# Optimization experiments

Measured on AMD Instinct MI355X. Metric: run time of the kernel, lower is better.

The kernel has to match this reference:

```python
import jax, jax.numpy as jnp
import numpy as np

B, T, D, A = 8, 256, 512, 512  # hidden dim D must equal attn size A per the TF code


def setup_inputs() -> dict:
    key = jax.random.key(0)
    ks = jax.random.split(key, 12)
    g = lambda k, shp, fan: jax.random.normal(k, shp, jnp.float32) * (1.0 / np.sqrt(fan))
    return {
        "state_outputs": jax.random.normal(ks[0], (B, T, D), jnp.float32),
        "final_state": jax.random.normal(ks[1], (B, D), jnp.float32),
        "intent_v": g(ks[2], (A,), A),
        "W_ih": g(ks[3], (D, A), D), "b_ih": jnp.zeros((A,), jnp.float32),
        "W_ii": g(ks[4], (D, A), D), "b_ii": jnp.zeros((A,), jnp.float32),
        "slot_v": g(ks[5], (A,), A),
        "W_sh": g(ks[6], (D, A), D), "b_sh": jnp.zeros((A,), jnp.float32),
        "W_si": g(ks[7], (D, A), D), "b_si": jnp.zeros((A,), jnp.float32),
    }


def reference(state_outputs, final_state, intent_v, W_ih, b_ih, W_ii, b_ii,
              slot_v, W_sh, b_sh, W_si, b_si):
    # ---- intent attention ----
    ih = jnp.einsum('btd,da->bta', state_outputs, W_ih) + b_ih        # [B,T,A]
    ii = final_state @ W_ii + b_ii                                     # [B,A]
    intent_score = jnp.sum(intent_v * jnp.tanh(ih + ii[:, None, :]), axis=-1)  # [B,T]
    intent_w = jax.nn.softmax(intent_score, axis=-1)
    c_intent = jnp.einsum('bt,btd->bd', intent_w, state_outputs)       # [B,D]

    # ---- slot attention ----
    sh = jnp.einsum('btd,da->bta', state_outputs, W_sh) + b_sh         # keys   [B,T,A]
    si = jnp.einsum('btd,da->bta', state_outputs, W_si) + b_si         # queries[B,T,A]
    # score[b,t,s] over pairs: tanh(sh[b,s] + si[b,t]) . slot_v
    slot_score = jnp.sum(slot_v * jnp.tanh(sh[:, None, :, :] + si[:, :, None, :]), axis=-1)  # [B,T,T]
    slot_w = jax.nn.softmax(slot_score, axis=-1)
    c_slot = jnp.einsum('bts,bsd->btd', slot_w, state_outputs)         # [B,T,D]
    return c_slot, c_intent
```

## Files before the change

kernel.cpp:

```cpp
#include <hip/hip_runtime.h>

#define BB 8
#define TT 256
#define DD 512
#define AA 512

#define PS 2.8853900817779268f
#define LOG2E 1.4426950408889634f

typedef __attribute__((ext_vector_type(8))) short short8;
typedef __attribute__((ext_vector_type(4))) float f32x4;

__device__ __forceinline__ float fast_tanh(float x) {
    float e = __builtin_amdgcn_exp2f(x * PS);
    float r = __builtin_amdgcn_rcpf(1.0f + e);
    return fmaf(-2.0f, r, 1.0f);
}

__device__ __forceinline__ ushort f2bf(float x) {
    uint u = __float_as_uint(x);
    uint r = (u + 0x7fffu + ((u >> 16) & 1u)) >> 16;
    return (ushort)r;
}
__device__ __forceinline__ float bf2f(ushort h) {
    return __uint_as_float(((uint)h) << 16);
}

__global__ __launch_bounds__(256) void prep(const float* __restrict__ SO,
                                            ushort* __restrict__ Ast,
                                            const float* __restrict__ Wsh,
                                            const float* __restrict__ Wsi,
                                            const float* __restrict__ Wih,
                                            ushort* __restrict__ Wt,
                                            const float* __restrict__ fs_g,
                                            const float* __restrict__ Wii,
                                            const float* __restrict__ bii,
                                            float* __restrict__ ii) {
    const int bid = blockIdx.x;
    const int tid = threadIdx.x;
    __shared__ float T[32][33];
    __shared__ float fs[DD];

    if (bid < 16) {
        int b = bid >> 1, half = bid & 1;
        int a = half * 256 + tid;
        fs[tid]       = fs_g[b * DD + tid];
        fs[tid + 256] = fs_g[b * DD + tid + 256];
        __syncthreads();
        float acc = bii[a];
        #pragma unroll 8
        for (int d = 0; d < DD; ++d)
            acc = fmaf(fs[d], Wii[(size_t)d * AA + a], acc);
        ii[b * AA + a] = acc;
    } else if (bid < 784) {
        int lbid = bid - 16;
        int z = lbid >> 8;
        int rem = lbid & 255;
        const float* W = (z == 0) ? Wsh : (z == 1) ? Wsi : Wih;
        int k0 = (rem & 15) * 32, n0 = (rem >> 4) * 32;
        int tx = tid & 31, ty = tid >> 5;
        #pragma unroll
        for (int r = 0; r < 4; ++r) {
            int kl = ty * 4 + r;
            T[kl][tx] = W[(size_t)(k0 + kl) * 512 + n0 + tx];
        }
        __syncthreads();
        size_t nbase = (size_t)z * 512 + n0;
        #pragma unroll
        for (int r = 0; r < 4; ++r) {
            int nl = ty * 4 + r;
            float v = T[tx][nl];
            ushort hi = f2bf(v);
            ushort lo = f2bf(v - bf2f(hi));
            Wt[(nbase + nl) * 1024 + k0 + tx]       = hi;
            Wt[(nbase + nl) * 1024 + 512 + k0 + tx] = lo;
        }
    } else {
        int qid = (bid - 784) * 256 + tid;
        int m = qid >> 7;
        int k4 = (qid & 127) * 4;
        float4 v = *reinterpret_cast<const float4*>(&SO[(size_t)m * 512 + k4]);
        ushort4 hi, lo;
        hi.x = f2bf(v.x); lo.x = f2bf(v.x - bf2f(hi.x));
        hi.y = f2bf(v.y); lo.y = f2bf(v.y - bf2f(hi.y));
        hi.z = f2bf(v.z); lo.z = f2bf(v.z - bf2f(hi.z));
        hi.w = f2bf(v.w); lo.w = f2bf(v.w - bf2f(hi.w));
        *reinterpret_cast<ushort4*>(&Ast[(size_t)m * 1024 + k4])       = hi;
        *reinterpret_cast<ushort4*>(&Ast[(size_t)m * 1024 + 512 + k4]) = lo;
    }
}

__global__ __launch_bounds__(256) void gemm_mfma(
    const ushort* __restrict__ Ast, const ushort* __restrict__ Wt,
    const float* __restrict__ bsh, const float* __restrict__ bsi,
    const float* __restrict__ bih,
    const float* __restrict__ ii, const float* __restrict__ iv,
    float* __restrict__ EhT, float* __restrict__ Es, float* __restrict__ ipart) {
    __shared__ __align__(16) ushort Al[2][128 * 32];
    __shared__ __align__(16) ushort Bl[2][128 * 32];
    const int tid = threadIdx.x;
    const int wave = tid >> 6, lane = tid & 63;
    const int wr = wave >> 1, wc = wave & 1;
    const int m0 = blockIdx.x * 128;
    const int by = blockIdx.y;
    const int l15 = lane & 15, kb = lane >> 4;

    f32x4 acc[4][4] = {};

    const char* Ab = reinterpret_cast<const char*>(Ast);
    const char* Bb = reinterpret_cast<const char*>(Wt);
    char* AlB = reinterpret_cast<char*>(&Al[0][0]);
    char* BlB = reinterpret_cast<char*>(&Bl[0][0]);

    const int srow  = tid >> 1;
    const int sslot = (tid & 1) * 2;
    const int swz   = (srow >> 1) & 3;
    const int lw0 = srow * 64 + ((sslot    ) ^ swz) * 16;
    const int lw1 = srow * 64 + ((sslot + 1) ^ swz) * 16;
    const char* agp = Ab + (size_t)(m0 + srow) * 2048 + sslot * 16;
    const char* bgp = Bb + (size_t)(by * 128 + srow) * 2048 + sslot * 16;

    int aro[4], bro[4];
    #pragma unroll
    for (int i = 0; i < 4; ++i) {
        int ra = wr * 64 + i * 16 + l15;
        aro[i] = ra * 64 + ((kb ^ ((ra >> 1) & 3)) * 16);
        int rb = wc * 64 + i * 16 + l15;
        bro[i] = rb * 64 + ((kb ^ ((rb >> 1) & 3)) * 16);
    }

    #define ABYTE(k0) (((k0) < 1024 ? (k0) : (k0) - 1024) * 2)
    #define BBYTE(k0) (((k0) < 512 ? (k0) : (k0) - 512) * 2)

    {
        short8 a0 = *reinterpret_cast<const short8*>(agp + ABYTE(0));
        short8 a1 = *reinterpret_cast<const short8*>(agp + ABYTE(0) + 16);
        short8 b0 = *reinterpret_cast<const short8*>(bgp + BBYTE(0));
        short8 b1 = *reinterpret_cast<const short8*>(bgp + BBYTE(0) + 16);
        *reinterpret_cast<short8*>(AlB + lw0) = a0;
        *reinterpret_cast<short8*>(AlB + lw1) = a1;
        *reinterpret_cast<short8*>(BlB + lw0) = b0;
        *reinterpret_cast<short8*>(BlB + lw1) = b1;
    }
    __syncthreads();

    int cur = 0;
    for (int it = 0; it < 48; ++it) {
        short8 a0, a1, b0, b1;
        const bool pf = (it + 1 < 48);
        if (pf) {
            int k0 = (it + 1) * 32;
            int ab = ABYTE(k0), bb = BBYTE(k0);
            a0 = *reinterpret_cast<const short8*>(agp + ab);
            a1 = *reinterpret_cast<const short8*>(agp + ab + 16);
            b0 = *reinterpret_cast<const short8*>(bgp + bb);
            b1 = *reinterpret_cast<const short8*>(bgp + bb + 16);
        }
        const char* Ac = AlB + cur * 8192;
        const char* Bc = BlB + cur * 8192;
        short8 af[4], bf[4];
        #pragma unroll
        for (int i = 0; i < 4; ++i) {
            af[i] = *reinterpret_cast<const short8*>(Ac + aro[i]);
            bf[i] = *reinterpret_cast<const short8*>(Bc + bro[i]);
        }
        #pragma unroll
        for (int i = 0; i < 4; ++i)
            #pragma unroll
            for (int j = 0; j < 4; ++j)
                acc[i][j] = __builtin_amdgcn_mfma_f32_16x16x32_bf16(
                    af[i], bf[j], acc[i][j], 0, 0, 0);
        if (pf) {
            char* An = AlB + (cur ^ 1) * 8192;
            char* Bn = BlB + (cur ^ 1) * 8192;
            *reinterpret_cast<short8*>(An + lw0) = a0;
            *reinterpret_cast<short8*>(An + lw1) = a1;
            *reinterpret_cast<short8*>(Bn + lw0) = b0;
            *reinterpret_cast<short8*>(Bn + lw1) = b1;
        }
        __syncthreads();
        cur ^= 1;
    }

    const int b = m0 >> 8;
    const int region = by >> 2;
    if (region == 0) {
        #pragma unroll
        for (int i = 0; i < 4; ++i) {
            int t0 = (m0 & 255) + wr * 64 + i * 16 + kb * 4;
            #pragma unroll
            for (int j = 0; j < 4; ++j) {
                int n = by * 128 + wc * 64 + j * 16 + l15;
                float bbv = bsh[n];
                float4 v;
                v.x = __builtin_amdgcn_exp2f((acc[i][j][0] + bbv) * PS);
                v.y = __builtin_amdgcn_exp2f((acc[i][j][1] + bbv) * PS);
                v.z = __builtin_amdgcn_exp2f((acc[i][j][2] + bbv) * PS);
                v.w = __builtin_amdgcn_exp2f((acc[i][j][3] + bbv) * PS);
                *reinterpret_cast<float4*>(&EhT[((size_t)b * 512 + n) * 256 + t0]) = v;
            }
        }
    } else if (region == 1) {
        #pragma unroll
        for (int i = 0; i < 4; ++i) {
            #pragma unroll
            for (int j = 0; j < 4; ++j) {
                int n = (by - 4) * 128 + wc * 64 + j * 16 + l15;
                float bbv = bsi[n];
                #pragma unroll
                for (int r = 0; r < 4; ++r) {
                    int m = m0 + wr * 64 + i * 16 + kb * 4 + r;
                    Es[(size_t)m * 512 + n] = __builtin_amdgcn_exp2f((acc[i][j][r] + bbv) * PS);
                }
            }
        }
    } else {
        int slot = (by - 8) * 2 + wc;
        #pragma unroll
        for (int i = 0; i < 4; ++i) {
            float p0 = 0.f, p1 = 0.f, p2 = 0.f, p3 = 0.f;
            #pragma unroll
            for (int j = 0; j < 4; ++j) {
                int n = (by - 8) * 128 + wc * 64 + j * 16 + l15;
                float add = bih[n] + ii[b * 512 + n];
                float w = iv[n];
                p0 = fmaf(w, fast_tanh(acc[i][j][0] + add), p0);
                p1 = fmaf(w, fast_tanh(acc[i][j][1] + add), p1);
                p2 = fmaf(w, fast_tanh(acc[i][j][2] + add), p2);
                p3 = fmaf(w, fast_tanh(acc[i][j][3] + add), p3);
            }
            #pragma unroll
            for (int off = 1; off < 16; off <<= 1) {
                p0 += __shfl_xor(p0, off);
                p1 += __shfl_xor(p1, off);
                p2 += __shfl_xor(p2, off);
                p3 += __shfl_xor(p3, off);
            }
            int mb = m0 + wr * 64 + i * 16 + kb * 4;
            if (l15 == 0) ipart[slot * 2048 + mb + 0] = p0;
            if (l15 == 1) ipart[slot * 2048 + mb + 1] = p1;
            if (l15 == 2) ipart[slot * 2048 + mb + 2] = p2;
            if (l15 == 3) ipart[slot * 2048 + mb + 3] = p3;
        }
    }
}

#define TS 64
#define KS 16
#define LPAD 72

__global__ __launch_bounds__(256) void k0_ii(const float* __restrict__ fs_g,
                                             const float* __restrict__ Wii,
                                             const float* __restrict__ bii,
                                             float* __restrict__ ii) {
    int b = blockIdx.x, tid = threadIdx.x;
    int a = blockIdx.y * 256 + tid;
    __shared__ float fs[DD];
    fs[tid]       = fs_g[b * DD + tid];
    fs[tid + 256] = fs_g[b * DD + tid + 256];
    __syncthreads();
    float acc = bii[a];
    #pragma unroll 8
    for (int d = 0; d < DD; ++d)
        acc = fmaf(fs[d], Wii[(size_t)d * AA + a], acc);
    ii[b * AA + a] = acc;
}

__global__ __launch_bounds__(256) void k1_gemm_old(
    const float* __restrict__ SO,
    const float* __restrict__ Wsh, const float* __restrict__ bsh,
    const float* __restrict__ Wsi, const float* __restrict__ bsi,
    const float* __restrict__ Wih, const float* __restrict__ bih,
    const float* __restrict__ ii, const float* __restrict__ iv,
    float* __restrict__ EhT, float* __restrict__ Es, float* __restrict__ ipart) {
    const int mode = blockIdx.z;
    const float* W;
    const float* bias;
    if (mode == 0)      { W = Wsh; bias = bsh; }
    else if (mode == 1) { W = Wsi; bias = bsi; }
    else                { W = Wih; bias = bih; }

    const int m0 = blockIdx.x * TS;
    const int n0 = blockIdx.y * TS;
    const int tid = threadIdx.x;
    const int tx = tid & 15, ty = tid >> 4;

    __shared__ __align__(16) float As[KS][LPAD];
    __shared__ __align__(16) float Bs[KS][LPAD];
    __shared__ __align__(16) float Cs[TS][LPAD];

    float acc[4][4] = {};
    const int arow = tid >> 2;
    const int akc  = (tid & 3) * 4;
    const int brw  = tid >> 4;
    const int bnc  = (tid & 15) * 4;

    for (int k0 = 0; k0 < DD; k0 += KS) {
        float4 av = *reinterpret_cast<const float4*>(&SO[(m0 + arow) * DD + k0 + akc]);
        As[akc + 0][arow] = av.x;
        As[akc + 1][arow] = av.y;
        As[akc + 2][arow] = av.z;
        As[akc + 3][arow] = av.w;
        float4 bv = *reinterpret_cast<const float4*>(&W[(k0 + brw) * AA + n0 + bnc]);
        *reinterpret_cast<float4*>(&Bs[brw][bnc]) = bv;
        __syncthreads();
        #pragma unroll
        for (int kk = 0; kk < KS; ++kk) {
            float4 a4 = *reinterpret_cast<const float4*>(&As[kk][ty * 4]);
            float4 b4 = *reinterpret_cast<const float4*>(&Bs[kk][tx * 4]);
            float av_[4] = {a4.x, a4.y, a4.z, a4.w};
            float bv_[4] = {b4.x, b4.y, b4.z, b4.w};
            #pragma unroll
            for (int i = 0; i < 4; ++i)
                #pragma unroll
                for (int j = 0; j < 4; ++j)
                    acc[i][j] = fmaf(av_[i], bv_[j], acc[i][j]);
        }
        __syncthreads();
    }

    if (mode == 1) {
        #pragma unroll
        for (int i = 0; i < 4; ++i) {
            int m = m0 + ty * 4 + i;
            float4 v;
            v.x = __builtin_amdgcn_exp2f((acc[i][0] + bias[n0 + tx * 4 + 0]) * PS);
            v.y = __builtin_amdgcn_exp2f((acc[i][1] + bias[n0 + tx * 4 + 1]) * PS);
            v.z = __builtin_amdgcn_exp2f((acc[i][2] + bias[n0 + tx * 4 + 2]) * PS);
            v.w = __builtin_amdgcn_exp2f((acc[i][3] + bias[n0 + tx * 4 + 3]) * PS);
            *reinterpret_cast<float4*>(&Es[(size_t)m * AA + n0 + tx * 4]) = v;
        }
    } else if (mode == 0) {
        #pragma unroll
        for (int i = 0; i < 4; ++i)
            #pragma unroll
            for (int j = 0; j < 4; ++j)
                Cs[tx * 4 + j][ty * 4 + i] =
                    __builtin_amdgcn_exp2f((acc[i][j] + bias[n0 + tx * 4 + j]) * PS);
        __syncthreads();
        int row = tid >> 2, part = tid & 3;
        int bb = m0 >> 8;
        int tstart = (m0 & 255) + part * 16;
        float* dst = &EhT[bb * (AA * TT) + (n0 + row) * TT + tstart];
        #pragma unroll
        for (int q = 0; q < 4; ++q) {
            float4 v = *reinterpret_cast<const float4*>(&Cs[row][part * 16 + q * 4]);
            *reinterpret_cast<float4*>(&dst[q * 4]) = v;
        }
    } else {
        int bb = m0 >> 8;
        #pragma unroll
        for (int i = 0; i < 4; ++i) {
            float p = 0.f;
            #pragma unroll
            for (int j = 0; j < 4; ++j) {
                int n = n0 + tx * 4 + j;
                float x = acc[i][j] + bias[n] + ii[bb * AA + n];
                p = fmaf(iv[n], fast_tanh(x), p);
            }
            Cs[ty * 4 + i][tx] = p;
        }
        __syncthreads();
        if (tid < 64) {
            float s = 0.f;
            #pragma unroll
            for (int k = 0; k < 16; ++k) s += Cs[tid][k];
            ipart[blockIdx.y * 2048 + m0 + tid] = s;
        }
    }
}

__global__ __launch_bounds__(512) void k3_fused(const float* __restrict__ SO,
                                                const float* __restrict__ EhT,
                                                const float* __restrict__ Es,
                                                const float* __restrict__ sv_g,
                                                const float* __restrict__ ipart,
                                                float* __restrict__ out_cslot,
                                                float* __restrict__ out_cint,
                                                int npart) {
    const int bid = blockIdx.x;
    const int tid = threadIdx.x;

    __shared__ __align__(16) float est[512][4];
    __shared__ __align__(16) float sv[512];
    __shared__ __align__(8)  float yp[4][4][256];
    __shared__ __align__(16) float wlt[256][4];
    __shared__ float redm[4][2];
    __shared__ float reds[4][2];
    __shared__ float redI[256];
    __shared__ float wlI[256];

    if (bid >= 8) {
        const int sb_ = bid - 8;
        const int b = sb_ & 7;
        const int t0 = (sb_ >> 3) * 4;
        const int sp = tid & 127;
        const int ah = tid >> 7;
        const int abase = ah * 128;

        {
            const float* esrc = &Es[(size_t)(b * 256 + t0) * 512];
            #pragma unroll
            for (int i = tid; i < 2048; i += 512) est[i & 511][i >> 9] = esrc[i];
            sv[tid] = sv_g[tid];
        }
        __syncthreads();

        const float* hp = &EhT[((size_t)b * 512 + abase) * 256 + 2 * sp];
        float a00=0.f,a01=0.f,a10=0.f,a11=0.f,a20=0.f,a21=0.f,a30=0.f,a31=0.f;
        for (int a0 = 0; a0 < 128; a0 += 4) {
            float4 v4 = *reinterpret_cast<const float4*>(&sv[abase + a0]);
            float2 h[4];
            #pragma unroll
            for (int u = 0; u < 4; ++u)
                h[u] = *reinterpret_cast<const float2*>(&hp[(a0 + u) * 256]);
            #pragma unroll
            for (int u = 0; u < 4; ++u) {
                float4 e4 = *reinterpret_cast<const float4*>(&est[abase + a0 + u][0]);
                float vv = (u == 0) ? v4.x : (u == 1) ? v4.y : (u == 2) ? v4.z : v4.w;
                float hx = h[u].x, hy = h[u].y;
                a00 = fmaf(vv, __builtin_amdgcn_rcpf(fmaf(hx, e4.x, 1.f)), a00);
                a01 = fmaf(vv, __builtin_amdgcn_rcpf(fmaf(hy, e4.x, 1.f)), a01);
                a10 = fmaf(vv, __builtin_amdgcn_rcpf(fmaf(hx, e4.y, 1.f)), a10);
                a11 = fmaf(vv, __builtin_amdgcn_rcpf(fmaf(hy, e4.y, 1.f)), a11);
                a20 = fmaf(vv, __builtin_amdgcn_rcpf(fmaf(hx, e4.z, 1.f)), a20);
                a21 = fmaf(vv, __builtin_amdgcn_rcpf(fmaf(hy, e4.z, 1.f)), a21);
                a30 = fmaf(vv, __builtin_amdgcn_rcpf(fmaf(hx, e4.w, 1.f)), a30);
                a31 = fmaf(vv, __builtin_amdgcn_rcpf(fmaf(hy, e4.w, 1.f)), a31);
            }
        }
        *reinterpret_cast<float2*>(&yp[ah][0][2 * sp]) = make_float2(a00, a01);
        *reinterpret_cast<float2*>(&yp[ah][1][2 * sp]) = make_float2(a10, a11);
        *reinterpret_cast<float2*>(&yp[ah][2][2 * sp]) = make_float2(a20, a21);
        *reinterpret_cast<float2*>(&yp[ah][3][2 * sp]) = make_float2(a30, a31);
        __syncthreads();

        const int g = ah;
        const int L = sp;
        const int w2 = (tid >> 6) & 1;
        float yL = (yp[0][g][L]       + yp[1][g][L])       + (yp[2][g][L]       + yp[3][g][L]);
        float yH = (yp[0][g][L + 128] + yp[1][g][L + 128]) + (yp[2][g][L + 128] + yp[3][g][L + 128]);
        float mn = fminf(yL, yH);
        #pragma unroll
        for (int off = 1; off < 64; off <<= 1)
            mn = fminf(mn, __shfl_xor(mn, off));
        if ((tid & 63) == 0) redm[g][w2] = mn;
        __syncthreads();
        mn = fminf(redm[g][0], redm[g][1]);
        float eL = __builtin_amdgcn_exp2f(PS * (mn - yL));
        float eH = __builtin_amdgcn_exp2f(PS * (mn - yH));
        float sm = eL + eH;
        #pragma unroll
        for (int off = 1; off < 64; off <<= 1)
            sm += __shfl_xor(sm, off);
        if ((tid & 63) == 0) reds[g][w2] = sm;
        __syncthreads();
        sm = reds[g][0] + reds[g][1];
        float rs = __builtin_amdgcn_rcpf(sm);
        wlt[L][g]       = eL * rs;
        wlt[L + 128][g] = eH * rs;
        __syncthreads();

        const int d = tid;
        const float* sop = &SO[(size_t)b * 256 * 512 + d];
        float c0 = 0.f, c1 = 0.f, c2 = 0.f, c3 = 0.f;
        for (int s0 = 0; s0 < 256; s0 += 4) {
            float so[4];
            #pragma unroll
            for (int u = 0; u < 4; ++u) so[u] = sop[(s0 + u) * 512];
            #pragma unroll
            for (int u = 0; u < 4; ++u) {
                float4 w4 = *reinterpret_cast<const float4*>(&wlt[s0 + u][0]);
                c0 = fmaf(w4.x, so[u], c0);
                c1 = fmaf(w4.y, so[u], c1);
                c2 = fmaf(w4.z, so[u], c2);
                c3 = fmaf(w4.w, so[u], c3);
            }
        }
        float* op = &out_cslot[((size_t)(b * 256 + t0)) * 512 + d];
        op[0] = c0; op[512] = c1; op[1024] = c2; op[1536] = c3;
    } else {
        const int b = bid;
        float sc = 0.f;
        if (tid < 256) {
            for (int nb = 0; nb < npart; ++nb) sc += ipart[nb * 2048 + b * 256 + tid];
            redI[tid] = sc;
        }
        __syncthreads();
        for (int off = 128; off > 0; off >>= 1) {
            if (tid < off) redI[tid] = fmaxf(redI[tid], redI[tid + off]);
            __syncthreads();
        }
        float mx = redI[0];
        __syncthreads();
        float e = 0.f;
        if (tid < 256) { e = __builtin_amdgcn_exp2f((sc - mx) * LOG2E); redI[tid] = e; }
        __syncthreads();
        for (int off = 128; off > 0; off >>= 1) {
            if (tid < off) redI[tid] += redI[tid + off];
            __syncthreads();
        }
        if (tid < 256) wlI[tid] = e * __builtin_amdgcn_rcpf(redI[0]);
        __syncthreads();
        const int d = tid;
        float c = 0.f;
        const float* sop = &SO[(size_t)b * 256 * 512 + d];
        for (int s0 = 0; s0 < 256; s0 += 4) {
            float so[4];
            #pragma unroll
            for (int u = 0; u < 4; ++u) so[u] = sop[(s0 + u) * 512];
            #pragma unroll
            for (int u = 0; u < 4; ++u) c = fmaf(wlI[s0 + u], so[u], c);
        }
        out_cint[(size_t)b * 512 + d] = c;
    }
}

extern "C" void kernel_launch(void* const* d_in, const int* in_sizes, int n_in,
                              void* d_out, int out_size, void* d_ws, size_t ws_size,
                              hipStream_t stream) {
    const float* SO  = (const float*)d_in[0];
    const float* FS  = (const float*)d_in[1];
    const float* IV  = (const float*)d_in[2];
    const float* Wih = (const float*)d_in[3];
    const float* bih = (const float*)d_in[4];
    const float* Wii = (const float*)d_in[5];
    const float* bii = (const float*)d_in[6];
    const float* SV  = (const float*)d_in[7];
    const float* Wsh = (const float*)d_in[8];
    const float* bsh = (const float*)d_in[9];
    const float* Wsi = (const float*)d_in[10];
    const float* bsi = (const float*)d_in[11];

    float* ws    = (float*)d_ws;
    float* EhT   = ws;
    float* Es    = ws + 1048576;
    float* ii    = ws + 2097152;
    float* ipart = ws + 2101248;
    ushort* Ast  = (ushort*)(ws + 2134016);
    ushort* Wt   = (ushort*)(ws + 3182592);
    const size_t NEED = (size_t)3969024 * 4;

    float* out_cslot = (float*)d_out;
    float* out_cint  = out_cslot + BB * TT * DD;

    if (ws_size >= NEED) {
        prep<<<1808, 256, 0, stream>>>(SO, Ast, Wsh, Wsi, Wih, Wt, FS, Wii, bii, ii);
        gemm_mfma<<<dim3(16, 12), 256, 0, stream>>>(Ast, Wt, bsh, bsi, bih, ii, IV,
                                                    EhT, Es, ipart);
        k3_fused<<<520, 512, 0, stream>>>(SO, EhT, Es, SV, ipart, out_cslot, out_cint, 8);
    } else {
        k0_ii<<<dim3(BB, 2), 256, 0, stream>>>(FS, Wii, bii, ii);
        k1_gemm_old<<<dim3(32, 8, 3), 256, 0, stream>>>(SO, Wsh, bsh, Wsi, bsi, Wih, bih,
                                                        ii, IV, EhT, Es, ipart);
        k3_fused<<<520, 512, 0, stream>>>(SO, EhT, Es, SV, ipart, out_cslot, out_cint, 8);
    }
}
```

Baseline: 104.5 us.

## Shrink GEMM tiles to 64x64, fold intent softmax into slot blocks, prefetch EhT

The MFMA GEMM moves from 128x128 tiles with K-step 32 to 64x64 tiles with K-step 64, raising the grid from 192 to 768 blocks so more CUs are busy. This changes the LDS swizzle and the intent partial-sum slot count (npart becomes 16). The fused attention kernel drops its 8 dedicated intent blocks: the first 8 slot blocks also run the intent softmax after their own work, which trims the grid to 512. The slot-score loop now double-buffers the EhT loads so global reads overlap the rcp/FMA work. Smaller tiles mean less data reuse per block and more redundant global traffic, and blocks 0-7 now carry extra serial work.

```diff
diff --git a/kernel.cpp b/kernel.cpp
--- a/kernel.cpp
+++ b/kernel.cpp
@@ -25,6 +25,9 @@
 __device__ __forceinline__ float bf2f(ushort h) {
     return __uint_as_float(((uint)h) << 16);
 }
+
+#define ABYTE(k0) (((k0) < 1024 ? (k0) : (k0) - 1024) * 2)
+#define BBYTE(k0) (((k0) < 512 ? (k0) : (k0) - 512) * 2)
 
 __global__ __launch_bounds__(256) void prep(const float* __restrict__ SO,
                                             ushort* __restrict__ Ast,
@@ -96,47 +99,46 @@
     const float* __restrict__ bih,
     const float* __restrict__ ii, const float* __restrict__ iv,
     float* __restrict__ EhT, float* __restrict__ Es, float* __restrict__ ipart) {
-    __shared__ __align__(16) ushort Al[2][128 * 32];
-    __shared__ __align__(16) ushort Bl[2][128 * 32];
+    __shared__ __align__(16) ushort Al[2][64 * 64];
+    __shared__ __align__(16) ushort Bl[2][64 * 64];
     const int tid = threadIdx.x;
     const int wave = tid >> 6, lane = tid & 63;
     const int wr = wave >> 1, wc = wave & 1;
-    const int m0 = blockIdx.x * 128;
+    const int m0 = blockIdx.x * 64;
     const int by = blockIdx.y;
+    const int n0 = by * 64;
     const int l15 = lane & 15, kb = lane >> 4;
 
-    f32x4 acc[4][4] = {};
+    f32x4 acc[2][2] = {};
 
     const char* Ab = reinterpret_cast<const char*>(Ast);
     const char* Bb = reinterpret_cast<const char*>(Wt);
     char* AlB = reinterpret_cast<char*>(&Al[0][0]);
     char* BlB = reinterpret_cast<char*>(&Bl[0][0]);
 
-    const int srow  = tid >> 1;
-    const int sslot = (tid & 1) * 2;
-    const int swz   = (srow >> 1) & 3;
-    const int lw0 = srow * 64 + ((sslot    ) ^ swz) * 16;
-    const int lw1 = srow * 64 + ((sslot + 1) ^ swz) * 16;
+    const int srow = tid >> 2, sslot = tid & 3;
+    const int lw0 = srow * 128 + (((sslot    ) ^ (srow & 7)) * 16);
+    const int lw1 = srow * 128 + (((sslot + 4) ^ (srow & 7)) * 16);
     const char* agp = Ab + (size_t)(m0 + srow) * 2048 + sslot * 16;
-    const char* bgp = Bb + (size_t)(by * 128 + srow) * 2048 + sslot * 16;
-
-    int aro[4], bro[4];
+    const char* bgp = Bb + (size_t)(n0 + srow) * 2048 + sslot * 16;
+
+    int aro[2][2], bro[2][2];
     #pragma unroll
-    for (int i = 0; i < 4; ++i) {
-        int ra = wr * 64 + i * 16 + l15;
-        aro[i] = ra * 64 + ((kb ^ ((ra >> 1) & 3)) * 16);
-        int rb = wc * 64 + i * 16 + l15;
-        bro[i] = rb * 64 + ((kb ^ ((rb >> 1) & 3)) * 16);
-    }
-
-    #define ABYTE(k0) (((k0) < 1024 ? (k0) : (k0) - 1024) * 2)
-    #define BBYTE(k0) (((k0) < 512 ? (k0) : (k0) - 512) * 2)
+    for (int i = 0; i < 2; ++i) {
+        int ra = wr * 32 + i * 16 + l15;
+        int rb = wc * 32 + i * 16 + l15;
+        #pragma unroll
+        for (int kk = 0; kk < 2; ++kk) {
+            aro[kk][i] = ra * 128 + (((kk * 4 + kb) ^ (ra & 7)) * 16);
+            bro[kk][i] = rb * 128 + (((kk * 4 + kb) ^ (rb & 7)) * 16);
+        }
+    }
 
     {
         short8 a0 = *reinterpret_cast<const short8*>(agp + ABYTE(0));
-        short8 a1 = *reinterpret_cast<const short8*>(agp + ABYTE(0) + 16);
+        short8 a1 = *reinterpret_cast<const short8*>(agp + ABYTE(0) + 64);
         short8 b0 = *reinterpret_cast<const short8*>(bgp + BBYTE(0));
-        short8 b1 = *reinterpret_cast<const short8*>(bgp + BBYTE(0) + 16);
+        short8 b1 = *reinterpret_cast<const short8*>(bgp + BBYTE(0) + 64);
         *reinterpret_cast<short8*>(AlB + lw0) = a0;
         *reinterpret_cast<short8*>(AlB + lw1) = a1;
         *reinterpret_cast<short8*>(BlB + lw0) = b0;
@@ -145,52 +147,54 @@
     __syncthreads();
 
     int cur = 0;
-    for (int it = 0; it < 48; ++it) {
-        short8 a0, a1, b0, b1;
-        const bool pf = (it + 1 < 48);
+    for (int it = 0; it < 24; ++it) {
+        short8 pa0, pa1, pb0, pb1;
+        const bool pf = (it + 1 < 24);
         if (pf) {
-            int k0 = (it + 1) * 32;
+            int k0 = (it + 1) * 64;
             int ab = ABYTE(k0), bb = BBYTE(k0);
-            a0 = *reinterpret_cast<const short8*>(agp + ab);
-            a1 = *reinterpret_cast<const short8*>(agp + ab + 16);
-            b0 = *reinterpret_cast<const short8*>(bgp + bb);
-            b1 = *reinterpret_cast<const short8*>(bgp + bb + 16);
+            pa0 = *reinterpret_cast<const short8*>(agp + ab);
+            pa1 = *reinterpret_cast<const short8*>(agp + ab + 64);
+            pb0 = *reinterpret_cast<const short8*>(bgp + bb);
+            pb1 = *reinterpret_cast<const short8*>(bgp + bb + 64);
         }
         const char* Ac = AlB + cur * 8192;
         const char* Bc = BlB + cur * 8192;
-        short8 af[4], bf[4];
-        #pragma unroll
-        for (int i = 0; i < 4; ++i) {
-            af[i] = *reinterpret_cast<const short8*>(Ac + aro[i]);
-            bf[i] = *reinterpret_cast<const short8*>(Bc + bro[i]);
-        }
-        #pragma unroll
-        for (int i = 0; i < 4; ++i)
-            #pragma unroll
-            for (int j = 0; j < 4; ++j)
-                acc[i][j] = __builtin_amdgcn_mfma_f32_16x16x32_bf16(
-                    af[i], bf[j], acc[i][j], 0, 0, 0);
+        #pragma unroll
+        for (int kk = 0; kk < 2; ++kk) {
+            short8 af[2], bf[2];
+            #pragma unroll
+            for (int i = 0; i < 2; ++i) {
+                af[i] = *reinterpret_cast<const short8*>(Ac + aro[kk][i]);
+                bf[i] = *reinterpret_cast<const short8*>(Bc + bro[kk][i]);
+            }
+            #pragma unroll
+            for (int i = 0; i < 2; ++i)
+                #pragma unroll
+                for (int j = 0; j < 2; ++j)
+                    acc[i][j] = __builtin_amdgcn_mfma_f32_16x16x32_bf16(
+                        af[i], bf[j], acc[i][j], 0, 0, 0);
+        }
         if (pf) {
             char* An = AlB + (cur ^ 1) * 8192;
             char* Bn = BlB + (cur ^ 1) * 8192;
-            *reinterpret_cast<short8*>(An + lw0) = a0;
-            *reinterpret_cast<short8*>(An + lw1) = a1;
-            *reinterpret_cast<short8*>(Bn + lw0) = b0;
-            *reinterpret_cast<short8*>(Bn + lw1) = b1;
+            *reinterpret_cast<short8*>(An + lw0) = pa0;
+            *reinterpret_cast<short8*>(An + lw1) = pa1;
+            *reinterpret_cast<short8*>(Bn + lw0) = pb0;
+            *reinterpret_cast<short8*>(Bn + lw1) = pb1;
         }
         __syncthreads();
         cur ^= 1;
     }
 
     const int b = m0 >> 8;
-    const int region = by >> 2;
-    if (region == 0) {
-        #pragma unroll
-        for (int i = 0; i < 4; ++i) {
-            int t0 = (m0 & 255) + wr * 64 + i * 16 + kb * 4;
-            #pragma unroll
-            for (int j = 0; j < 4; ++j) {
-                int n = by * 128 + wc * 64 + j * 16 + l15;
+    if (by < 8) {
+        #pragma unroll
+        for (int i = 0; i < 2; ++i) {
+            int t0 = (m0 & 255) + wr * 32 + i * 16 + kb * 4;
+            #pragma unroll
+            for (int j = 0; j < 2; ++j) {
+                int n = n0 + wc * 32 + j * 16 + l15;
                 float bbv = bsh[n];
                 float4 v;
                 v.x = __builtin_amdgcn_exp2f((acc[i][j][0] + bbv) * PS);
@@ -200,28 +204,28 @@
                 *reinterpret_cast<float4*>(&EhT[((size_t)b * 512 + n) * 256 + t0]) = v;
             }
         }
-    } else if (region == 1) {
-        #pragma unroll
-        for (int i = 0; i < 4; ++i) {
-            #pragma unroll
-            for (int j = 0; j < 4; ++j) {
-                int n = (by - 4) * 128 + wc * 64 + j * 16 + l15;
+    } else if (by < 16) {
+        #pragma unroll
+        for (int i = 0; i < 2; ++i) {
+            #pragma unroll
+            for (int j = 0; j < 2; ++j) {
+                int n = n0 - 512 + wc * 32 + j * 16 + l15;
                 float bbv = bsi[n];
                 #pragma unroll
                 for (int r = 0; r < 4; ++r) {
-                    int m = m0 + wr * 64 + i * 16 + kb * 4 + r;
+                    int m = m0 + wr * 32 + i * 16 + kb * 4 + r;
                     Es[(size_t)m * 512 + n] = __builtin_amdgcn_exp2f((acc[i][j][r] + bbv) * PS);
                 }
             }
         }
     } else {
-        int slot = (by - 8) * 2 + wc;
-        #pragma unroll
-        for (int i = 0; i < 4; ++i) {
+        int slot = (by - 16) * 2 + wc;
+        #pragma unroll
+        for (int i = 0; i < 2; ++i) {
             float p0 = 0.f, p1 = 0.f, p2 = 0.f, p3 = 0.f;
             #pragma unroll
-            for (int j = 0; j < 4; ++j) {
-                int n = (by - 8) * 128 + wc * 64 + j * 16 + l15;
+            for (int j = 0; j < 2; ++j) {
+                int n = n0 - 1024 + wc * 32 + j * 16 + l15;
                 float add = bih[n] + ii[b * 512 + n];
                 float w = iv[n];
                 p0 = fmaf(w, fast_tanh(acc[i][j][0] + add), p0);
@@ -236,7 +240,7 @@
                 p2 += __shfl_xor(p2, off);
                 p3 += __shfl_xor(p3, off);
             }
-            int mb = m0 + wr * 64 + i * 16 + kb * 4;
+            int mb = m0 + wr * 32 + i * 16 + kb * 4;
             if (l15 == 0) ipart[slot * 2048 + mb + 0] = p0;
             if (l15 == 1) ipart[slot * 2048 + mb + 1] = p1;
             if (l15 == 2) ipart[slot * 2048 + mb + 2] = p2;
@@ -390,51 +394,63 @@
     __shared__ float redI[256];
     __shared__ float wlI[256];
 
-    if (bid >= 8) {
-        const int sb_ = bid - 8;
-        const int b = sb_ & 7;
-        const int t0 = (sb_ >> 3) * 4;
-        const int sp = tid & 127;
-        const int ah = tid >> 7;
-        const int abase = ah * 128;
-
-        {
-            const float* esrc = &Es[(size_t)(b * 256 + t0) * 512];
-            #pragma unroll
-            for (int i = tid; i < 2048; i += 512) est[i & 511][i >> 9] = esrc[i];
-            sv[tid] = sv_g[tid];
-        }
-        __syncthreads();
-
-        const float* hp = &EhT[((size_t)b * 512 + abase) * 256 + 2 * sp];
-        float a00=0.f,a01=0.f,a10=0.f,a11=0.f,a20=0.f,a21=0.f,a30=0.f,a31=0.f;
-        for (int a0 = 0; a0 < 128; a0 += 4) {
-            float4 v4 = *reinterpret_cast<const float4*>(&sv[abase + a0]);
-            float2 h[4];
-            #pragma unroll
-            for (int u = 0; u < 4; ++u)
-                h[u] = *reinterpret_cast<const float2*>(&hp[(a0 + u) * 256]);
-            #pragma unroll
-            for (int u = 0; u < 4; ++u) {
-                float4 e4 = *reinterpret_cast<const float4*>(&est[abase + a0 + u][0]);
-                float vv = (u == 0) ? v4.x : (u == 1) ? v4.y : (u == 2) ? v4.z : v4.w;
-                float hx = h[u].x, hy = h[u].y;
-                a00 = fmaf(vv, __builtin_amdgcn_rcpf(fmaf(hx, e4.x, 1.f)), a00);
-                a01 = fmaf(vv, __builtin_amdgcn_rcpf(fmaf(hy, e4.x, 1.f)), a01);
-                a10 = fmaf(vv, __builtin_amdgcn_rcpf(fmaf(hx, e4.y, 1.f)), a10);
-                a11 = fmaf(vv, __builtin_amdgcn_rcpf(fmaf(hy, e4.y, 1.f)), a11);
-                a20 = fmaf(vv, __builtin_amdgcn_rcpf(fmaf(hx, e4.z, 1.f)), a20);
-                a21 = fmaf(vv, __builtin_amdgcn_rcpf(fmaf(hy, e4.z, 1.f)), a21);
-                a30 = fmaf(vv, __builtin_amdgcn_rcpf(fmaf(hx, e4.w, 1.f)), a30);
-                a31 = fmaf(vv, __builtin_amdgcn_rcpf(fmaf(hy, e4.w, 1.f)), a31);
-            }
-        }
-        *reinterpret_cast<float2*>(&yp[ah][0][2 * sp]) = make_float2(a00, a01);
-        *reinterpret_cast<float2*>(&yp[ah][1][2 * sp]) = make_float2(a10, a11);
-        *reinterpret_cast<float2*>(&yp[ah][2][2 * sp]) = make_float2(a20, a21);
-        *reinterpret_cast<float2*>(&yp[ah][3][2 * sp]) = make_float2(a30, a31);
-        __syncthreads();
-
+    const int b = bid & 7;
+    const int t0 = (bid >> 3) * 4;
+    const int sp = tid & 127;
+    const int ah = tid >> 7;
+    const int abase = ah * 128;
+
+    {
+        const float* esrc = &Es[(size_t)(b * 256 + t0) * 512];
+        #pragma unroll
+        for (int i = tid; i < 2048; i += 512) est[i & 511][i >> 9] = esrc[i];
+        sv[tid] = sv_g[tid];
+    }
+    __syncthreads();
+
+    const float* hp = &EhT[((size_t)b * 512 + abase) * 256 + 2 * sp];
+    float a00=0.f,a01=0.f,a10=0.f,a11=0.f,a20=0.f,a21=0.f,a30=0.f,a31=0.f;
+    float2 h0[4], h1[4];
+    #pragma unroll
+    for (int u = 0; u < 4; ++u)
+        h0[u] = *reinterpret_cast<const float2*>(&hp[u * 256]);
+
+    #define SCORE4(A0, H) do {                                                         \
+        float4 v4 = *reinterpret_cast<const float4*>(&sv[abase + (A0)]);               \
+        _Pragma("unroll")                                                              \
+        for (int u = 0; u < 4; ++u) {                                                  \
+            float4 e4 = *reinterpret_cast<const float4*>(&est[abase + (A0) + u][0]);   \
+            float vv = (u == 0) ? v4.x : (u == 1) ? v4.y : (u == 2) ? v4.z : v4.w;     \
+            float hx = H[u].x, hy = H[u].y;                                            \
+            a00 = fmaf(vv, __builtin_amdgcn_rcpf(fmaf(hx, e4.x, 1.f)), a00);           \
+            a01 = fmaf(vv, __builtin_amdgcn_rcpf(fmaf(hy, e4.x, 1.f)), a01);           \
+            a10 = fmaf(vv, __builtin_amdgcn_rcpf(fmaf(hx, e4.y, 1.f)), a10);           \
+            a11 = fmaf(vv, __builtin_amdgcn_rcpf(fmaf(hy, e4.y, 1.f)), a11);           \
+            a20 = fmaf(vv, __builtin_amdgcn_rcpf(fmaf(hx, e4.z, 1.f)), a20);           \
+            a21 = fmaf(vv, __builtin_amdgcn_rcpf(fmaf(hy, e4.z, 1.f)), a21);           \
+            a30 = fmaf(vv, __builtin_amdgcn_rcpf(fmaf(hx, e4.w, 1.f)), a30);           \
+            a31 = fmaf(vv, __builtin_amdgcn_rcpf(fmaf(hy, e4.w, 1.f)), a31);           \
+        }                                                                              \
+    } while (0)
+
+    for (int a0 = 0; a0 < 128; a0 += 8) {
+        #pragma unroll
+        for (int u = 0; u < 4; ++u)
+            h1[u] = *reinterpret_cast<const float2*>(&hp[(a0 + 4 + u) * 256]);
+        SCORE4(a0, h0);
+        #pragma unroll
+        for (int u = 0; u < 4; ++u)
+            h0[u] = *reinterpret_cast<const float2*>(&hp[(a0 + 8 + u) * 256]);
+        SCORE4(a0 + 4, h1);
+    }
+
+    *reinterpret_cast<float2*>(&yp[ah][0][2 * sp]) = make_float2(a00, a01);
+    *reinterpret_cast<float2*>(&yp[ah][1][2 * sp]) = make_float2(a10, a11);
+    *reinterpret_cast<float2*>(&yp[ah][2][2 * sp]) = make_float2(a20, a21);
+    *reinterpret_cast<float2*>(&yp[ah][3][2 * sp]) = make_float2(a30, a31);
+    __syncthreads();
+
+    {
         const int g = ah;
         const int L = sp;
         const int w2 = (tid >> 6) & 1;
@@ -459,8 +475,10 @@
         float rs = __builtin_amdgcn_rcpf(sm);
         wlt[L][g]       = eL * rs;
         wlt[L + 128][g] = eH * rs;
-        __syncthreads();
-
+    }
+    __syncthreads();
+
+    {
         const int d = tid;
         const float* sop = &SO[(size_t)b * 256 * 512 + d];
         float c0 = 0.f, c1 = 0.f, c2 = 0.f, c3 = 0.f;
@@ -479,8 +497,10 @@
         }
         float* op = &out_cslot[((size_t)(b * 256 + t0)) * 512 + d];
         op[0] = c0; op[512] = c1; op[1024] = c2; op[1536] = c3;
-    } else {
-        const int b = bid;
+    }
+
+    if (bid < 8) {
+        __syncthreads();
         float sc = 0.f;
         if (tid < 256) {
             for (int nb = 0; nb < npart; ++nb) sc += ipart[nb * 2048 + b * 256 + tid];
@@ -546,13 +566,13 @@
 
     if (ws_size >= NEED) {
         prep<<<1808, 256, 0, stream>>>(SO, Ast, Wsh, Wsi, Wih, Wt, FS, Wii, bii, ii);
-        gemm_mfma<<<dim3(16, 12), 256, 0, stream>>>(Ast, Wt, bsh, bsi, bih, ii, IV,
+        gemm_mfma<<<dim3(32, 24), 256, 0, stream>>>(Ast, Wt, bsh, bsi, bih, ii, IV,
                                                     EhT, Es, ipart);
-        k3_fused<<<520, 512, 0, stream>>>(SO, EhT, Es, SV, ipart, out_cslot, out_cint, 8);
+        k3_fused<<<512, 512, 0, stream>>>(SO, EhT, Es, SV, ipart, out_cslot, out_cint, 16);
     } else {
         k0_ii<<<dim3(BB, 2), 256, 0, stream>>>(FS, Wii, bii, ii);
         k1_gemm_old<<<dim3(32, 8, 3), 256, 0, stream>>>(SO, Wsh, bsh, Wsi, bsi, Wih, bih,
                                                         ii, IV, EhT, Es, ipart);
-        k3_fused<<<520, 512, 0, stream>>>(SO, EhT, Es, SV, ipart, out_cslot, out_cint, 8);
-    }
-}
+        k3_fused<<<512, 512, 0, stream>>>(SO, EhT, Es, SV, ipart, out_cslot, out_cint, 8);
+    }
+}
```

Result: faster. 93.33 us (-10.7%).
